# Kernel tuning notes

Measured on AMD Instinct MI355X. Metric: run time of the kernel, lower is better.

## Reference

```python
import jax, jax.numpy as jnp
import numpy as np

EPS = 1e-5

def _layer_norm(x, g, b):
    m = jnp.mean(x, axis=-1, keepdims=True)
    v = jnp.mean((x - m) ** 2, axis=-1, keepdims=True)
    return (x - m) / jnp.sqrt(v + EPS) * g + b

def _dpb(idx, w0, b0, g1, be1, w1, b1, g2, be2, w2, b2, g3, be3, w3, b3):
    # idx: (n, dim, 1) -> (h, n, dim)
    h = idx @ w0 + b0                                   # (n, dim, D)
    h = jax.nn.relu(_layer_norm(h, g1, be1)) @ w1 + b1  # pos1
    h = jax.nn.relu(_layer_norm(h, g2, be2)) @ w2 + b2  # pos2
    h = jax.nn.relu(_layer_norm(h, g3, be3)) @ w3 + b3  # pos3 -> (n, dim, H)
    return jnp.transpose(h, (2, 0, 1))                  # (H, n, dim)

def setup_inputs() -> dict:
    key = jax.random.key(0)
    ks = jax.random.split(key, 6)
    B, H, N, DIM, D = 8, 16, 4096, 64, 64
    s = 0.02
    return {
        "x": jax.random.normal(ks[0], (B, H, N, DIM), jnp.float32),
        "w0": jax.random.normal(ks[1], (1, D), jnp.float32) * s,
        "b0": jnp.zeros((D,), jnp.float32),
        "g1": jnp.ones((D,), jnp.float32),
        "be1": jnp.zeros((D,), jnp.float32),
        "w1": jax.random.normal(ks[2], (D, D), jnp.float32) * s,
        "b1": jnp.zeros((D,), jnp.float32),
        "g2": jnp.ones((D,), jnp.float32),
        "be2": jnp.zeros((D,), jnp.float32),
        "w2": jax.random.normal(ks[3], (D, D), jnp.float32) * s,
        "b2": jnp.zeros((D,), jnp.float32),
        "g3": jnp.ones((D,), jnp.float32),
        "be3": jnp.zeros((D,), jnp.float32),
        "w3": jax.random.normal(ks[4], (D, H), jnp.float32) * s,
        "b3": jnp.zeros((H,), jnp.float32),
    }

def reference(x, w0, b0, g1, be1, w1, b1, g2, be2, w2, b2, g3, be3, w3, b3):
    # DynamicToepliztMultiheadV3 forward (par_type=1, no pad/exp/decay, non-causal)
    n = x.shape[-2]
    dim = x.shape[-1]
    m = n - 1
    dpb_args = (w0, b0, g1, be1, w1, b1, g2, be2, w2, b2, g3, be3, w3, b3)
    scale = 1.0 / (m * dim)
    flat = jnp.arange(1, 1 + m * dim, dtype=x.dtype)
    pos_idx = (flat * scale).reshape(m, dim, 1)
    neg_idx = (-jnp.flip(flat) * scale).reshape(m, dim, 1)  # flip on flat, then reshape (matches torch)
    zero_idx = jnp.zeros((1, dim, 1), x.dtype)
    zero = _dpb(zero_idx, *dpb_args)   # (H, 1, dim)
    pos = _dpb(pos_idx, *dpb_args)     # (H, n-1, dim)
    neg = _dpb(neg_idx, *dpb_args)     # (H, n-1, dim)
    a = jnp.concatenate([zero, pos, zero, neg], axis=1)  # (H, 2n, dim)
    # FFT-based circular (Toeplitz) convolution along seq axis
    y = jnp.fft.rfft(x, 2 * n, axis=-2, norm='ortho')          # (B,H,n+1,dim) complex
    v = jnp.fft.rfft(a, axis=-2)[None]                          # backward norm, as in torch
    out = jnp.fft.irfft(v * y, 2 * n, axis=-2, norm='ortho')[:, :, :n, :]
    return out
```

## Files before the change

kernel.cpp:

```cpp
#include <hip/hip_runtime.h>
#include <math.h>

static const size_t OFF_TW = 0;
static const size_t OFF_V  = 32768;
static const size_t OFF_AT = OFF_V  + (size_t)16 * 64 * 4104 * 8;
static const size_t OFF_ZX = OFF_AT + (size_t)16 * 32 * 8192 * 8;
static const size_t WS_NEED = OFF_ZX + (size_t)128 * 32 * 4096 * 8;

__global__ void __launch_bounds__(256) k_init_tw(float2* __restrict__ tw)
{
    int k = blockIdx.x * 256 + threadIdx.x;
    if (k < 4096) {
        double a = (double)k * (3.14159265358979323846 / 4096.0);
        tw[k] = make_float2((float)cos(a), (float)(-sin(a)));
    }
}

__device__ __forceinline__ void ln_relu_arr(float* b,
                                            const float* __restrict__ g,
                                            const float* __restrict__ be)
{
    float s0 = 0, s1 = 0, s2 = 0, s3 = 0;
    #pragma unroll
    for (int k = 0; k < 64; k += 4) {
        s0 += b[k]; s1 += b[k + 1]; s2 += b[k + 2]; s3 += b[k + 3];
    }
    float m = (s0 + s1 + s2 + s3) * (1.0f / 64.0f);
    float v0 = 0, v1 = 0, v2 = 0, v3 = 0;
    #pragma unroll
    for (int k = 0; k < 64; k += 4) {
        float c0 = b[k] - m, c1 = b[k + 1] - m, c2 = b[k + 2] - m, c3 = b[k + 3] - m;
        v0 = fmaf(c0, c0, v0); v1 = fmaf(c1, c1, v1);
        v2 = fmaf(c2, c2, v2); v3 = fmaf(c3, c3, v3);
    }
    float inv = rsqrtf((v0 + v1 + v2 + v3) * (1.0f / 64.0f) + 1e-5f);
    #pragma unroll
    for (int k = 0; k < 64; ++k)
        b[k] = fmaxf(fmaf((b[k] - m) * inv, g[k], be[k]), 0.0f);
}

__device__ __forceinline__ void matmul64(const float* b, float* o,
                                         const float* __restrict__ w,
                                         const float* __restrict__ bias)
{
    #pragma unroll
    for (int j = 0; j < 64; ++j) o[j] = bias[j];
    #pragma unroll
    for (int k = 0; k < 64; ++k) {
        float bk = b[k];
        const float* wr = w + (k << 6);
        #pragma unroll
        for (int j = 0; j < 64; ++j) o[j] = fmaf(bk, wr[j], o[j]);
    }
}

__global__ void __launch_bounds__(256) k_dpb(
    const float* __restrict__ w0,  const float* __restrict__ b0,
    const float* __restrict__ g1,  const float* __restrict__ be1,
    const float* __restrict__ w1,  const float* __restrict__ b1,
    const float* __restrict__ g2,  const float* __restrict__ be2,
    const float* __restrict__ w2,  const float* __restrict__ b2,
    const float* __restrict__ g3,  const float* __restrict__ be3,
    const float* __restrict__ w3,  const float* __restrict__ b3,
    float* __restrict__ aTf)
{
    int e  = blockIdx.x * 256 + threadIdx.x;
    int r  = e & 8191;
    int dd = e >> 13;
    const float scale = (float)(1.0 / 262080.0);
    float u;
    if (r == 0 || r == 4096) u = 0.0f;
    else if (r < 4096)       u = (float)((r - 1) * 64 + dd + 1) * scale;
    else                     u = -(float)(262080 - ((r - 4097) * 64 + dd)) * scale;

    float b[64], o[64];
    #pragma unroll
    for (int j = 0; j < 64; ++j) b[j] = fmaf(u, w0[j], b0[j]);

    ln_relu_arr(b, g1, be1);
    matmul64(b, o, w1, b1);
    ln_relu_arr(o, g2, be2);
    matmul64(o, b, w2, b2);
    ln_relu_arr(b, g3, be3);

    float f[16];
    #pragma unroll
    for (int j = 0; j < 16; ++j) f[j] = b3[j];
    #pragma unroll
    for (int k = 0; k < 64; ++k) {
        float bk = b[k];
        const float* wr = w3 + (k << 4);
        #pragma unroll
        for (int j = 0; j < 16; ++j) f[j] = fmaf(bk, wr[j], f[j]);
    }
    #pragma unroll
    for (int h = 0; h < 16; ++h) {
        size_t idx = ((size_t)((h << 5) + (dd >> 1)) * 8192 + r) * 2 + (dd & 1);
        aTf[idx] = f[h];
    }
}

__device__ __forceinline__ int sw(int a)
{
    return a ^ ((a >> 4) & 15) ^ ((a >> 8) & 1);
}

__device__ __forceinline__ float2 cmul(float2 a, float2 b)
{
    return make_float2(fmaf(a.x, b.x, -(a.y * b.y)), fmaf(a.x, b.y, a.y * b.x));
}

template<bool INV>
__device__ __forceinline__ float2 twm(float2 a, float wr, float wi)
{
    float i = INV ? -wi : wi;
    return make_float2(fmaf(a.x, wr, -(a.y * i)), fmaf(a.x, i, a.y * wr));
}

template<bool INV>
__device__ __forceinline__ void fft8(float2* z)
{
    const float SQ = 0.70710678118654752440f;
    #pragma unroll
    for (int b = 0; b < 8; b += 2) {
        float2 u = z[b], t = z[b + 1];
        z[b]     = make_float2(u.x + t.x, u.y + t.y);
        z[b + 1] = make_float2(u.x - t.x, u.y - t.y);
    }
    const float w4r[2] = {1.0f, 0.0f};
    const float w4i[2] = {0.0f, -1.0f};
    #pragma unroll
    for (int b = 0; b < 8; b += 4) {
        #pragma unroll
        for (int j = 0; j < 2; ++j) {
            float2 u = z[b + j];
            float2 t = twm<INV>(z[b + j + 2], w4r[j], w4i[j]);
            z[b + j]     = make_float2(u.x + t.x, u.y + t.y);
            z[b + j + 2] = make_float2(u.x - t.x, u.y - t.y);
        }
    }
    const float w8r[4] = {1.0f, SQ, 0.0f, -SQ};
    const float w8i[4] = {0.0f, -SQ, -1.0f, -SQ};
    #pragma unroll
    for (int j = 0; j < 4; ++j) {
        float2 u = z[j];
        float2 t = twm<INV>(z[j + 4], w8r[j], w8i[j]);
        z[j]     = make_float2(u.x + t.x, u.y + t.y);
        z[j + 4] = make_float2(u.x - t.x, u.y - t.y);
    }
}

template<bool INV>
__device__ __forceinline__ void r8(float2* __restrict__ Z, int base, int j, int L, int s,
                                   const float2* __restrict__ tw)
{
    int addr[8];
    #pragma unroll
    for (int m = 0; m < 8; ++m) addr[m] = sw(base + j + L * m);
    float2 t1 = tw[j * s], t2 = tw[2 * j * s], t4 = tw[4 * j * s];
    if (INV) { t1.y = -t1.y; t2.y = -t2.y; t4.y = -t4.y; }
    float2 T3 = cmul(t1, t2), T5 = cmul(t1, t4), T6 = cmul(t2, t4), T7 = cmul(T3, t4);
    float2 z[8];
    z[0] = Z[addr[0]];
    z[1] = cmul(Z[addr[1]], t4);
    z[2] = cmul(Z[addr[2]], t2);
    z[3] = cmul(Z[addr[3]], T6);
    z[4] = cmul(Z[addr[4]], t1);
    z[5] = cmul(Z[addr[5]], T5);
    z[6] = cmul(Z[addr[6]], T3);
    z[7] = cmul(Z[addr[7]], T7);
    fft8<INV>(z);
    #pragma unroll
    for (int q = 0; q < 8; ++q) Z[addr[q]] = z[q];
}

template<int L, bool INV>
__device__ __forceinline__ void reg_stage16(float* xr, float* xi,
                                            const float2* __restrict__ tw)
{
    #pragma unroll
    for (int b = 0; b < 16; b += 2 * L) {
        #pragma unroll
        for (int j = 0; j < L; ++j) {
            float2 w = tw[j * (4096 / L)];
            float wr = w.x, wi = INV ? -w.y : w.y;
            int i0 = b + j, i1 = b + j + L;
            float tr = xr[i1] * wr - xi[i1] * wi;
            float ti = xr[i1] * wi + xi[i1] * wr;
            xr[i1] = xr[i0] - tr; xi[i1] = xi[i0] - ti;
            xr[i0] += tr;         xi[i0] += ti;
        }
    }
}

template<bool INV>
__device__ __forceinline__ void fft8192_lds(float2* __restrict__ Z,
                                            const float2* __restrict__ tw)
{
    const int t  = threadIdx.x;
    const int r9 = (int)(__brev((unsigned)t) >> 23);
    float xr[16], xi[16];
    #pragma unroll
    for (int i = 0; i < 16; ++i) {
        int r4 = (int)(__brev((unsigned)i) >> 28);
        float2 v = Z[sw((r4 << 9) | r9)];
        xr[i] = v.x; xi[i] = v.y;
    }
    __syncthreads();
    reg_stage16<1, INV>(xr, xi, tw);
    reg_stage16<2, INV>(xr, xi, tw);
    reg_stage16<4, INV>(xr, xi, tw);
    reg_stage16<8, INV>(xr, xi, tw);
    #pragma unroll
    for (int i = 0; i < 16; ++i) Z[sw(16 * t + i)] = make_float2(xr[i], xi[i]);
    __syncthreads();
    r8<INV>(Z, (t >> 4) * 128, t & 15, 16, 64, tw);
    r8<INV>(Z, ((t + 512) >> 4) * 128, t & 15, 16, 64, tw);
    __syncthreads();
    r8<INV>(Z, (t >> 7) * 1024, t & 127, 128, 8, tw);
    r8<INV>(Z, ((t + 512) >> 7) * 1024, (t + 512) & 127, 128, 8, tw);
    __syncthreads();
    r8<INV>(Z, 0, t, 1024, 1, tw);
    r8<INV>(Z, 0, t + 512, 1024, 1, tw);
    __syncthreads();
}

__global__ void __launch_bounds__(512, 4) k_vfft(const float2* __restrict__ aT,
                                                 const float2* __restrict__ tw,
                                                 float2* __restrict__ V)
{
    __shared__ float2 Z[8192];
    int blk = blockIdx.x;
    int h = blk >> 5, p = blk & 31;
    const float2* ac = aT + (size_t)(h * 32 + p) * 8192;
    int t = threadIdx.x;
    #pragma unroll
    for (int i = 0; i < 16; ++i) {
        int idx = i * 512 + t;
        Z[sw(idx)] = ac[idx];
    }
    __syncthreads();
    fft8192_lds<false>(Z, tw);
    const float s = 1.0f / 8192.0f;
    float2* V0 = V + (size_t)(h * 64 + 2 * p) * 4104;
    float2* V1 = V0 + 4104;
    for (int k = t; k <= 4096; k += 512) {
        int km = (8192 - k) & 8191;
        float2 z1 = Z[sw(k)], z2 = Z[sw(km)];
        float zr1 = z1.x, zi1 = z1.y;
        float zr2 = z2.x, zi2 = -z2.y;
        float a0r = 0.5f * (zr1 + zr2), a0i = 0.5f * (zi1 + zi2);
        float a1r = 0.5f * (zi1 - zi2), a1i = -0.5f * (zr1 - zr2);
        V0[k] = make_float2(a0r * s, a0i * s);
        V1[k] = make_float2(a1r * s, a1i * s);
    }
}

__global__ void __launch_bounds__(256) k_pack_x(const float* __restrict__ x,
                                                float2* __restrict__ zx)
{
    int blk = blockIdx.x;
    int bh = blk >> 7, rt = blk & 127, r0 = rt << 5;
    __shared__ float tile[64][33];
    const float* xp = x + (size_t)bh * 4096 * 64;
    int tid = threadIdx.x;
    #pragma unroll
    for (int i = 0; i < 8; ++i) {
        int idx = i * 256 + tid;
        int rr = idx >> 6, d = idx & 63;
        tile[d][rr] = xp[(size_t)(r0 + rr) * 64 + d];
    }
    __syncthreads();
    float2* zp = zx + (size_t)bh * 32 * 4096;
    #pragma unroll
    for (int i = 0; i < 4; ++i) {
        int idx = i * 256 + tid;
        int p = idx >> 5, rr = idx & 31;
        zp[(size_t)p * 4096 + r0 + rr] = make_float2(tile[2 * p][rr], tile[2 * p + 1][rr]);
    }
}

__global__ void __launch_bounds__(512, 4) k_conv(float2* __restrict__ zx,
                                                 const float2* __restrict__ V,
                                                 const float2* __restrict__ tw)
{
    __shared__ float2 Z[8192];
    int blk = blockIdx.x;
    int bh = blk >> 5, p = blk & 31, h = bh & 15;
    float2* zc = zx + (size_t)blk * 4096;
    int t = threadIdx.x;
    #pragma unroll
    for (int i = 0; i < 8; ++i) {
        int idx = i * 512 + t;
        Z[sw(idx)] = zc[idx];
        Z[sw(idx + 4096)] = make_float2(0.0f, 0.0f);
    }
    __syncthreads();
    fft8192_lds<false>(Z, tw);
    const float2* V0 = V + (size_t)(h * 64 + 2 * p) * 4104;
    const float2* V1 = V0 + 4104;
    for (int k = t; k <= 4096; k += 512) {
        int km = (8192 - k) & 8191;
        float2 z1 = Z[sw(k)], z2 = Z[sw(km)];
        float zr1 = z1.x, zi1 = z1.y;
        float zr2 = z2.x, zi2 = -z2.y;
        float x0r = 0.5f * (zr1 + zr2), x0i = 0.5f * (zi1 + zi2);
        float x1r = 0.5f * (zi1 - zi2), x1i = -0.5f * (zr1 - zr2);
        float2 v0 = V0[k], v1 = V1[k];
        float y0r = v0.x * x0r - v0.y * x0i, y0i = v0.x * x0i + v0.y * x0r;
        float y1r = v1.x * x1r - v1.y * x1i, y1i = v1.x * x1i + v1.y * x1r;
        Z[sw(k)] = make_float2(y0r - y1i, y0i + y1r);
        if (k > 0 && k < 4096)
            Z[sw(km)] = make_float2(y0r + y1i, y1r - y0i);
    }
    __syncthreads();
    fft8192_lds<true>(Z, tw);
    #pragma unroll
    for (int i = 0; i < 8; ++i) {
        int idx = i * 512 + t;
        zc[idx] = Z[sw(idx)];
    }
}

__global__ void __launch_bounds__(256) k_unpack_out(const float2* __restrict__ zo,
                                                    float* __restrict__ out)
{
    int blk = blockIdx.x;
    int bh = blk >> 7, rt = blk & 127, r0 = rt << 5;
    __shared__ float tile[64][33];
    const float2* zp = zo + (size_t)bh * 32 * 4096;
    int tid = threadIdx.x;
    #pragma unroll
    for (int i = 0; i < 4; ++i) {
        int idx = i * 256 + tid;
        int p = idx >> 5, rr = idx & 31;
        float2 v = zp[(size_t)p * 4096 + r0 + rr];
        tile[2 * p][rr] = v.x; tile[2 * p + 1][rr] = v.y;
    }
    __syncthreads();
    float* op = out + (size_t)bh * 4096 * 64;
    #pragma unroll
    for (int i = 0; i < 8; ++i) {
        int idx = i * 256 + tid;
        int rr = idx >> 6, d = idx & 63;
        op[(size_t)(r0 + rr) * 64 + d] = tile[d][rr];
    }
}

extern "C" void kernel_launch(void* const* d_in, const int* in_sizes, int n_in,
                              void* d_out, int out_size, void* d_ws, size_t ws_size,
                              hipStream_t stream)
{
    (void)in_sizes; (void)n_in; (void)out_size;
    const float* x   = (const float*)d_in[0];
    const float* w0  = (const float*)d_in[1];
    const float* b0  = (const float*)d_in[2];
    const float* g1  = (const float*)d_in[3];
    const float* be1 = (const float*)d_in[4];
    const float* w1  = (const float*)d_in[5];
    const float* b1  = (const float*)d_in[6];
    const float* g2  = (const float*)d_in[7];
    const float* be2 = (const float*)d_in[8];
    const float* w2  = (const float*)d_in[9];
    const float* b2  = (const float*)d_in[10];
    const float* g3  = (const float*)d_in[11];
    const float* be3 = (const float*)d_in[12];
    const float* w3  = (const float*)d_in[13];
    const float* b3  = (const float*)d_in[14];
    float* out = (float*)d_out;
    char* ws = (char*)d_ws;
    if (ws_size < WS_NEED) return;

    float2* tw = (float2*)(ws + OFF_TW);
    float2* V  = (float2*)(ws + OFF_V);
    float2* aT = (float2*)(ws + OFF_AT);
    float2* zx = (float2*)(ws + OFF_ZX);

    k_init_tw<<<16, 256, 0, stream>>>(tw);
    k_dpb<<<2048, 256, 0, stream>>>(w0, b0, g1, be1, w1, b1, g2, be2,
                                    w2, b2, g3, be3, w3, b3, (float*)aT);
    k_vfft<<<512, 512, 0, stream>>>(aT, tw, V);
    k_pack_x<<<16384, 256, 0, stream>>>(x, zx);
    k_conv<<<4096, 512, 0, stream>>>(zx, V, tw);
    k_unpack_out<<<16384, 256, 0, stream>>>((const float2*)zx, out);
}
```

Measured before the change: 779.5 us.

## Restructure 8192-point LDS FFT for 1024 threads and exploit zero padding

The in-LDS FFT is reworked from 512 threads with 16 register points each to 1024 threads with 8 register points each. It uses a new stage schedule: a radix-8 register pass, three radix-8 LDS passes, and a final radix-2 pass. In the forward conv FFT, the zero upper half is no longer written to shared memory. Instead, the first butterfly stage is skipped by duplicating the loaded values in registers. The goal is to cut LDS traffic and arithmetic and raise per-block parallelism, but launch_bounds(1024,1) may limit occupancy and changes register pressure.

```diff
diff --git a/kernel.cpp b/kernel.cpp
--- a/kernel.cpp
+++ b/kernel.cpp
@@ -175,11 +175,11 @@
 }
 
 template<int L, bool INV>
-__device__ __forceinline__ void reg_stage16(float* xr, float* xi,
-                                            const float2* __restrict__ tw)
-{
-    #pragma unroll
-    for (int b = 0; b < 16; b += 2 * L) {
+__device__ __forceinline__ void reg_stage8(float* xr, float* xi,
+                                           const float2* __restrict__ tw)
+{
+    #pragma unroll
+    for (int b = 0; b < 8; b += 2 * L) {
         #pragma unroll
         for (int j = 0; j < L; ++j) {
             float2 w = tw[j * (4096 / L)];
@@ -193,41 +193,60 @@
     }
 }
 
-template<bool INV>
+template<bool INV, bool PAD>
 __device__ __forceinline__ void fft8192_lds(float2* __restrict__ Z,
                                             const float2* __restrict__ tw)
 {
-    const int t  = threadIdx.x;
-    const int r9 = (int)(__brev((unsigned)t) >> 23);
-    float xr[16], xi[16];
-    #pragma unroll
-    for (int i = 0; i < 16; ++i) {
-        int r4 = (int)(__brev((unsigned)i) >> 28);
-        float2 v = Z[sw((r4 << 9) | r9)];
-        xr[i] = v.x; xi[i] = v.y;
-    }
-    __syncthreads();
-    reg_stage16<1, INV>(xr, xi, tw);
-    reg_stage16<2, INV>(xr, xi, tw);
-    reg_stage16<4, INV>(xr, xi, tw);
-    reg_stage16<8, INV>(xr, xi, tw);
-    #pragma unroll
-    for (int i = 0; i < 16; ++i) Z[sw(16 * t + i)] = make_float2(xr[i], xi[i]);
-    __syncthreads();
-    r8<INV>(Z, (t >> 4) * 128, t & 15, 16, 64, tw);
-    r8<INV>(Z, ((t + 512) >> 4) * 128, t & 15, 16, 64, tw);
-    __syncthreads();
-    r8<INV>(Z, (t >> 7) * 1024, t & 127, 128, 8, tw);
-    r8<INV>(Z, ((t + 512) >> 7) * 1024, (t + 512) & 127, 128, 8, tw);
-    __syncthreads();
-    r8<INV>(Z, 0, t, 1024, 1, tw);
-    r8<INV>(Z, 0, t + 512, 1024, 1, tw);
-    __syncthreads();
-}
-
-__global__ void __launch_bounds__(512, 4) k_vfft(const float2* __restrict__ aT,
-                                                 const float2* __restrict__ tw,
-                                                 float2* __restrict__ V)
+    const int t   = threadIdx.x;
+    const int r10 = (int)(__brev((unsigned)t) >> 22);
+    float xr[8], xi[8];
+    if (PAD) {
+        #pragma unroll
+        for (int i = 0; i < 8; i += 2) {
+            int r3 = (int)(__brev((unsigned)i) >> 29);
+            float2 v = Z[sw((r3 << 10) | r10)];
+            xr[i] = v.x; xi[i] = v.y;
+            xr[i + 1] = v.x; xi[i + 1] = v.y;
+        }
+    } else {
+        #pragma unroll
+        for (int i = 0; i < 8; ++i) {
+            int r3 = (int)(__brev((unsigned)i) >> 29);
+            float2 v = Z[sw((r3 << 10) | r10)];
+            xr[i] = v.x; xi[i] = v.y;
+        }
+    }
+    __syncthreads();
+    if (!PAD) reg_stage8<1, INV>(xr, xi, tw);
+    reg_stage8<2, INV>(xr, xi, tw);
+    reg_stage8<4, INV>(xr, xi, tw);
+    #pragma unroll
+    for (int i = 0; i < 8; ++i) Z[sw(8 * t + i)] = make_float2(xr[i], xi[i]);
+    __syncthreads();
+    r8<INV>(Z, (t >> 3) * 64, t & 7, 8, 128, tw);
+    __syncthreads();
+    r8<INV>(Z, (t >> 6) * 512, t & 63, 64, 16, tw);
+    __syncthreads();
+    r8<INV>(Z, (t >> 9) * 4096, t & 511, 512, 2, tw);
+    __syncthreads();
+    #pragma unroll
+    for (int m = 0; m < 4; ++m) {
+        int k = t + 1024 * m;
+        float2 w = tw[k];
+        float wi = INV ? -w.y : w.y;
+        int aL = sw(k), aH = sw(k + 4096);
+        float2 u = Z[aL], v = Z[aH];
+        float tr = fmaf(v.x, w.x, -(v.y * wi));
+        float ti = fmaf(v.x, wi, v.y * w.x);
+        Z[aL] = make_float2(u.x + tr, u.y + ti);
+        Z[aH] = make_float2(u.x - tr, u.y - ti);
+    }
+    __syncthreads();
+}
+
+__global__ void __launch_bounds__(1024, 1) k_vfft(const float2* __restrict__ aT,
+                                                  const float2* __restrict__ tw,
+                                                  float2* __restrict__ V)
 {
     __shared__ float2 Z[8192];
     int blk = blockIdx.x;
@@ -235,16 +254,16 @@
     const float2* ac = aT + (size_t)(h * 32 + p) * 8192;
     int t = threadIdx.x;
     #pragma unroll
-    for (int i = 0; i < 16; ++i) {
-        int idx = i * 512 + t;
+    for (int i = 0; i < 8; ++i) {
+        int idx = i * 1024 + t;
         Z[sw(idx)] = ac[idx];
     }
     __syncthreads();
-    fft8192_lds<false>(Z, tw);
+    fft8192_lds<false, false>(Z, tw);
     const float s = 1.0f / 8192.0f;
     float2* V0 = V + (size_t)(h * 64 + 2 * p) * 4104;
     float2* V1 = V0 + 4104;
-    for (int k = t; k <= 4096; k += 512) {
+    for (int k = t; k <= 4096; k += 1024) {
         int km = (8192 - k) & 8191;
         float2 z1 = Z[sw(k)], z2 = Z[sw(km)];
         float zr1 = z1.x, zi1 = z1.y;
@@ -280,9 +299,9 @@
     }
 }
 
-__global__ void __launch_bounds__(512, 4) k_conv(float2* __restrict__ zx,
-                                                 const float2* __restrict__ V,
-                                                 const float2* __restrict__ tw)
+__global__ void __launch_bounds__(1024, 1) k_conv(float2* __restrict__ zx,
+                                                  const float2* __restrict__ V,
+                                                  const float2* __restrict__ tw)
 {
     __shared__ float2 Z[8192];
     int blk = blockIdx.x;
@@ -290,16 +309,15 @@
     float2* zc = zx + (size_t)blk * 4096;
     int t = threadIdx.x;
     #pragma unroll
-    for (int i = 0; i < 8; ++i) {
-        int idx = i * 512 + t;
+    for (int i = 0; i < 4; ++i) {
+        int idx = i * 1024 + t;
         Z[sw(idx)] = zc[idx];
-        Z[sw(idx + 4096)] = make_float2(0.0f, 0.0f);
-    }
-    __syncthreads();
-    fft8192_lds<false>(Z, tw);
+    }
+    __syncthreads();
+    fft8192_lds<false, true>(Z, tw);
     const float2* V0 = V + (size_t)(h * 64 + 2 * p) * 4104;
     const float2* V1 = V0 + 4104;
-    for (int k = t; k <= 4096; k += 512) {
+    for (int k = t; k <= 4096; k += 1024) {
         int km = (8192 - k) & 8191;
         float2 z1 = Z[sw(k)], z2 = Z[sw(km)];
         float zr1 = z1.x, zi1 = z1.y;
@@ -314,10 +332,10 @@
             Z[sw(km)] = make_float2(y0r + y1i, y1r - y0i);
     }
     __syncthreads();
-    fft8192_lds<true>(Z, tw);
-    #pragma unroll
-    for (int i = 0; i < 8; ++i) {
-        int idx = i * 512 + t;
+    fft8192_lds<true, false>(Z, tw);
+    #pragma unroll
+    for (int i = 0; i < 4; ++i) {
+        int idx = i * 1024 + t;
         zc[idx] = Z[sw(idx)];
     }
 }
@@ -379,8 +397,8 @@
     k_init_tw<<<16, 256, 0, stream>>>(tw);
     k_dpb<<<2048, 256, 0, stream>>>(w0, b0, g1, be1, w1, b1, g2, be2,
                                     w2, b2, g3, be3, w3, b3, (float*)aT);
-    k_vfft<<<512, 512, 0, stream>>>(aT, tw, V);
+    k_vfft<<<512, 1024, 0, stream>>>(aT, tw, V);
     k_pack_x<<<16384, 256, 0, stream>>>(x, zx);
-    k_conv<<<4096, 512, 0, stream>>>(zx, V, tw);
+    k_conv<<<4096, 1024, 0, stream>>>(zx, V, tw);
     k_unpack_out<<<16384, 256, 0, stream>>>((const float2*)zx, out);
 }
```

New measurement: 770.7 us. About the same (-1.1%).

## Split 8192-point FFTs into even/odd 4096-point halves and stage DPB rows in LDS

Applied to the files above, without the earlier changes.

The 8192-point zero-padded FFTs in the convolution kernel become two 4096-point FFTs over the even and odd frequency bins. The odd-bin pass uses twiddle pre-multiplication, so the padded half is never transformed, and the inverse results are recombined with twiddles. This halves LDS use per block, though the kernel now runs four 4096-point FFTs and rereads its input. The V-spectrum kernel is split into even and odd blocks in the same way, and the DPB MLP stages activation rows in shared memory with smaller blocks to reduce register pressure.

```diff
diff --git a/kernel.cpp b/kernel.cpp
--- a/kernel.cpp
+++ b/kernel.cpp
@@ -39,22 +39,29 @@
         b[k] = fmaxf(fmaf((b[k] - m) * inv, g[k], be[k]), 0.0f);
 }
 
-__device__ __forceinline__ void matmul64(const float* b, float* o,
-                                         const float* __restrict__ w,
-                                         const float* __restrict__ bias)
-{
-    #pragma unroll
-    for (int j = 0; j < 64; ++j) o[j] = bias[j];
-    #pragma unroll
+__device__ __forceinline__ void store_row(float* __restrict__ row, const float* a)
+{
+    #pragma unroll
+    for (int k = 0; k < 64; ++k) row[k] = a[k];
+}
+
+template<int JN>
+__device__ __forceinline__ void matmul_lds(const float* __restrict__ row, float* o,
+                                           const float* __restrict__ w,
+                                           const float* __restrict__ bias)
+{
+    #pragma unroll
+    for (int j = 0; j < JN; ++j) o[j] = bias[j];
+    #pragma unroll 4
     for (int k = 0; k < 64; ++k) {
-        float bk = b[k];
-        const float* wr = w + (k << 6);
+        float bk = row[k];
+        const float* wr = w + k * JN;
         #pragma unroll
-        for (int j = 0; j < 64; ++j) o[j] = fmaf(bk, wr[j], o[j]);
-    }
-}
-
-__global__ void __launch_bounds__(256) k_dpb(
+        for (int j = 0; j < JN; ++j) o[j] = fmaf(bk, wr[j], o[j]);
+    }
+}
+
+__global__ void __launch_bounds__(128) k_dpb(
     const float* __restrict__ w0,  const float* __restrict__ b0,
     const float* __restrict__ g1,  const float* __restrict__ be1,
     const float* __restrict__ w1,  const float* __restrict__ b1,
@@ -64,7 +71,10 @@
     const float* __restrict__ w3,  const float* __restrict__ b3,
     float* __restrict__ aTf)
 {
-    int e  = blockIdx.x * 256 + threadIdx.x;
+    __shared__ float rowbuf[128 * 65];
+    float* row = &rowbuf[threadIdx.x * 65];
+
+    int e  = blockIdx.x * 128 + threadIdx.x;
     int r  = e & 8191;
     int dd = e >> 13;
     const float scale = (float)(1.0 / 262080.0);
@@ -73,26 +83,20 @@
     else if (r < 4096)       u = (float)((r - 1) * 64 + dd + 1) * scale;
     else                     u = -(float)(262080 - ((r - 4097) * 64 + dd)) * scale;
 
-    float b[64], o[64];
-    #pragma unroll
-    for (int j = 0; j < 64; ++j) b[j] = fmaf(u, w0[j], b0[j]);
-
-    ln_relu_arr(b, g1, be1);
-    matmul64(b, o, w1, b1);
+    float a[64], o[64];
+    #pragma unroll
+    for (int j = 0; j < 64; ++j) a[j] = fmaf(u, w0[j], b0[j]);
+    ln_relu_arr(a, g1, be1);
+    store_row(row, a);
+    matmul_lds<64>(row, o, w1, b1);
     ln_relu_arr(o, g2, be2);
-    matmul64(o, b, w2, b2);
-    ln_relu_arr(b, g3, be3);
-
+    store_row(row, o);
+    matmul_lds<64>(row, a, w2, b2);
+    ln_relu_arr(a, g3, be3);
+    store_row(row, a);
     float f[16];
-    #pragma unroll
-    for (int j = 0; j < 16; ++j) f[j] = b3[j];
-    #pragma unroll
-    for (int k = 0; k < 64; ++k) {
-        float bk = b[k];
-        const float* wr = w3 + (k << 4);
-        #pragma unroll
-        for (int j = 0; j < 16; ++j) f[j] = fmaf(bk, wr[j], f[j]);
-    }
+    matmul_lds<16>(row, f, w3, b3);
+
     #pragma unroll
     for (int h = 0; h < 16; ++h) {
         size_t idx = ((size_t)((h << 5) + (dd >> 1)) * 8192 + r) * 2 + (dd & 1);
@@ -175,11 +179,11 @@
 }
 
 template<int L, bool INV>
-__device__ __forceinline__ void reg_stage16(float* xr, float* xi,
-                                            const float2* __restrict__ tw)
-{
-    #pragma unroll
-    for (int b = 0; b < 16; b += 2 * L) {
+__device__ __forceinline__ void reg_stage8(float* xr, float* xi,
+                                           const float2* __restrict__ tw)
+{
+    #pragma unroll
+    for (int b = 0; b < 8; b += 2 * L) {
         #pragma unroll
         for (int j = 0; j < L; ++j) {
             float2 w = tw[j * (4096 / L)];
@@ -194,65 +198,81 @@
 }
 
 template<bool INV>
-__device__ __forceinline__ void fft8192_lds(float2* __restrict__ Z,
+__device__ __forceinline__ void fft4096_lds(float2* __restrict__ Z,
                                             const float2* __restrict__ tw)
 {
     const int t  = threadIdx.x;
     const int r9 = (int)(__brev((unsigned)t) >> 23);
-    float xr[16], xi[16];
-    #pragma unroll
-    for (int i = 0; i < 16; ++i) {
-        int r4 = (int)(__brev((unsigned)i) >> 28);
-        float2 v = Z[sw((r4 << 9) | r9)];
+    float xr[8], xi[8];
+    #pragma unroll
+    for (int i = 0; i < 8; ++i) {
+        int r3 = (int)(__brev((unsigned)i) >> 29);
+        float2 v = Z[sw((r3 << 9) | r9)];
         xr[i] = v.x; xi[i] = v.y;
     }
     __syncthreads();
-    reg_stage16<1, INV>(xr, xi, tw);
-    reg_stage16<2, INV>(xr, xi, tw);
-    reg_stage16<4, INV>(xr, xi, tw);
-    reg_stage16<8, INV>(xr, xi, tw);
-    #pragma unroll
-    for (int i = 0; i < 16; ++i) Z[sw(16 * t + i)] = make_float2(xr[i], xi[i]);
-    __syncthreads();
-    r8<INV>(Z, (t >> 4) * 128, t & 15, 16, 64, tw);
-    r8<INV>(Z, ((t + 512) >> 4) * 128, t & 15, 16, 64, tw);
-    __syncthreads();
-    r8<INV>(Z, (t >> 7) * 1024, t & 127, 128, 8, tw);
-    r8<INV>(Z, ((t + 512) >> 7) * 1024, (t + 512) & 127, 128, 8, tw);
-    __syncthreads();
-    r8<INV>(Z, 0, t, 1024, 1, tw);
-    r8<INV>(Z, 0, t + 512, 1024, 1, tw);
-    __syncthreads();
-}
-
-__global__ void __launch_bounds__(512, 4) k_vfft(const float2* __restrict__ aT,
+    reg_stage8<1, INV>(xr, xi, tw);
+    reg_stage8<2, INV>(xr, xi, tw);
+    reg_stage8<4, INV>(xr, xi, tw);
+    #pragma unroll
+    for (int i = 0; i < 8; ++i) Z[sw(8 * t + i)] = make_float2(xr[i], xi[i]);
+    __syncthreads();
+    r8<INV>(Z, (t >> 3) * 64, t & 7, 8, 128, tw);
+    __syncthreads();
+    r8<INV>(Z, (t >> 6) * 512, t & 63, 64, 16, tw);
+    __syncthreads();
+    r8<INV>(Z, 0, t, 512, 2, tw);
+    __syncthreads();
+}
+
+__global__ void __launch_bounds__(512, 3) k_vfft(const float2* __restrict__ aT,
                                                  const float2* __restrict__ tw,
                                                  float2* __restrict__ V)
 {
-    __shared__ float2 Z[8192];
+    __shared__ float2 Z[4096];
     int blk = blockIdx.x;
-    int h = blk >> 5, p = blk & 31;
-    const float2* ac = aT + (size_t)(h * 32 + p) * 8192;
+    int pair = blk >> 1, eo = blk & 1;
+    int h = pair >> 5, p = pair & 31;
+    const float2* ac = aT + (size_t)pair * 8192;
     int t = threadIdx.x;
-    #pragma unroll
-    for (int i = 0; i < 16; ++i) {
-        int idx = i * 512 + t;
-        Z[sw(idx)] = ac[idx];
-    }
-    __syncthreads();
-    fft8192_lds<false>(Z, tw);
+    if (eo == 0) {
+        #pragma unroll
+        for (int i = 0; i < 8; ++i) {
+            int idx = i * 512 + t;
+            float2 a = ac[idx], b = ac[idx + 4096];
+            Z[sw(idx)] = make_float2(a.x + b.x, a.y + b.y);
+        }
+    } else {
+        #pragma unroll
+        for (int i = 0; i < 8; ++i) {
+            int idx = i * 512 + t;
+            float2 a = ac[idx], b = ac[idx + 4096];
+            Z[sw(idx)] = cmul(make_float2(a.x - b.x, a.y - b.y), tw[idx]);
+        }
+    }
+    __syncthreads();
+    fft4096_lds<false>(Z, tw);
     const float s = 1.0f / 8192.0f;
     float2* V0 = V + (size_t)(h * 64 + 2 * p) * 4104;
     float2* V1 = V0 + 4104;
-    for (int k = t; k <= 4096; k += 512) {
-        int km = (8192 - k) & 8191;
-        float2 z1 = Z[sw(k)], z2 = Z[sw(km)];
-        float zr1 = z1.x, zi1 = z1.y;
-        float zr2 = z2.x, zi2 = -z2.y;
-        float a0r = 0.5f * (zr1 + zr2), a0i = 0.5f * (zi1 + zi2);
-        float a1r = 0.5f * (zi1 - zi2), a1i = -0.5f * (zr1 - zr2);
-        V0[k] = make_float2(a0r * s, a0i * s);
-        V1[k] = make_float2(a1r * s, a1i * s);
+    if (eo == 0) {
+        for (int j = t; j <= 2048; j += 512) {
+            int jm = (4096 - j) & 4095;
+            float2 z1 = Z[sw(j)], z2 = Z[sw(jm)];
+            float zr1 = z1.x, zi1 = z1.y;
+            float zr2 = z2.x, zi2 = -z2.y;
+            V0[2 * j] = make_float2(0.5f * (zr1 + zr2) * s, 0.5f * (zi1 + zi2) * s);
+            V1[2 * j] = make_float2(0.5f * (zi1 - zi2) * s, -0.5f * (zr1 - zr2) * s);
+        }
+    } else {
+        for (int j = t; j < 2048; j += 512) {
+            int jm = 4095 - j;
+            float2 z1 = Z[sw(j)], z2 = Z[sw(jm)];
+            float zr1 = z1.x, zi1 = z1.y;
+            float zr2 = z2.x, zi2 = -z2.y;
+            V0[2 * j + 1] = make_float2(0.5f * (zr1 + zr2) * s, 0.5f * (zi1 + zi2) * s);
+            V1[2 * j + 1] = make_float2(0.5f * (zi1 - zi2) * s, -0.5f * (zr1 - zr2) * s);
+        }
     }
 }
 
@@ -280,45 +300,79 @@
     }
 }
 
-__global__ void __launch_bounds__(512, 4) k_conv(float2* __restrict__ zx,
+__global__ void __launch_bounds__(512, 3) k_conv(float2* __restrict__ zx,
                                                  const float2* __restrict__ V,
                                                  const float2* __restrict__ tw)
 {
-    __shared__ float2 Z[8192];
+    __shared__ float2 Z[4096];
     int blk = blockIdx.x;
     int bh = blk >> 5, p = blk & 31, h = bh & 15;
     float2* zc = zx + (size_t)blk * 4096;
     int t = threadIdx.x;
+    const float2* V0 = V + (size_t)(h * 64 + 2 * p) * 4104;
+    const float2* V1 = V0 + 4104;
+
     #pragma unroll
     for (int i = 0; i < 8; ++i) {
         int idx = i * 512 + t;
         Z[sw(idx)] = zc[idx];
-        Z[sw(idx + 4096)] = make_float2(0.0f, 0.0f);
-    }
-    __syncthreads();
-    fft8192_lds<false>(Z, tw);
-    const float2* V0 = V + (size_t)(h * 64 + 2 * p) * 4104;
-    const float2* V1 = V0 + 4104;
-    for (int k = t; k <= 4096; k += 512) {
-        int km = (8192 - k) & 8191;
-        float2 z1 = Z[sw(k)], z2 = Z[sw(km)];
+    }
+    __syncthreads();
+    fft4096_lds<false>(Z, tw);
+    for (int j = t; j <= 2048; j += 512) {
+        int jm = (4096 - j) & 4095;
+        float2 z1 = Z[sw(j)], z2 = Z[sw(jm)];
         float zr1 = z1.x, zi1 = z1.y;
         float zr2 = z2.x, zi2 = -z2.y;
         float x0r = 0.5f * (zr1 + zr2), x0i = 0.5f * (zi1 + zi2);
         float x1r = 0.5f * (zi1 - zi2), x1i = -0.5f * (zr1 - zr2);
-        float2 v0 = V0[k], v1 = V1[k];
+        float2 v0 = V0[2 * j], v1 = V1[2 * j];
         float y0r = v0.x * x0r - v0.y * x0i, y0i = v0.x * x0i + v0.y * x0r;
         float y1r = v1.x * x1r - v1.y * x1i, y1i = v1.x * x1i + v1.y * x1r;
-        Z[sw(k)] = make_float2(y0r - y1i, y0i + y1r);
-        if (k > 0 && k < 4096)
-            Z[sw(km)] = make_float2(y0r + y1i, y1r - y0i);
-    }
-    __syncthreads();
-    fft8192_lds<true>(Z, tw);
+        Z[sw(j)] = make_float2(y0r - y1i, y0i + y1r);
+        if (j > 0 && j < 2048)
+            Z[sw(jm)] = make_float2(y0r + y1i, y1r - y0i);
+    }
+    __syncthreads();
+    fft4096_lds<true>(Z, tw);
+    float er[8], ei[8];
+    #pragma unroll
+    for (int i = 0; i < 8; ++i) {
+        float2 v = Z[sw(i * 512 + t)];
+        er[i] = v.x; ei[i] = v.y;
+    }
+    __syncthreads();
+
     #pragma unroll
     for (int i = 0; i < 8; ++i) {
         int idx = i * 512 + t;
-        zc[idx] = Z[sw(idx)];
+        Z[sw(idx)] = cmul(zc[idx], tw[idx]);
+    }
+    __syncthreads();
+    fft4096_lds<false>(Z, tw);
+    for (int j = t; j < 2048; j += 512) {
+        int jm = 4095 - j;
+        float2 z1 = Z[sw(j)], z2 = Z[sw(jm)];
+        float zr1 = z1.x, zi1 = z1.y;
+        float zr2 = z2.x, zi2 = -z2.y;
+        float x0r = 0.5f * (zr1 + zr2), x0i = 0.5f * (zi1 + zi2);
+        float x1r = 0.5f * (zi1 - zi2), x1i = -0.5f * (zr1 - zr2);
+        float2 v0 = V0[2 * j + 1], v1 = V1[2 * j + 1];
+        float y0r = v0.x * x0r - v0.y * x0i, y0i = v0.x * x0i + v0.y * x0r;
+        float y1r = v1.x * x1r - v1.y * x1i, y1i = v1.x * x1i + v1.y * x1r;
+        Z[sw(j)]  = make_float2(y0r - y1i, y0i + y1r);
+        Z[sw(jm)] = make_float2(y0r + y1i, y1r - y0i);
+    }
+    __syncthreads();
+    fft4096_lds<true>(Z, tw);
+    #pragma unroll
+    for (int i = 0; i < 8; ++i) {
+        int idx = i * 512 + t;
+        float2 o = Z[sw(idx)];
+        float2 w = tw[idx];
+        float yr = er[i] + (w.x * o.x + w.y * o.y);
+        float yi = ei[i] + (w.x * o.y - w.y * o.x);
+        zc[idx] = make_float2(yr, yi);
     }
 }
 
@@ -377,9 +431,9 @@
     float2* zx = (float2*)(ws + OFF_ZX);
 
     k_init_tw<<<16, 256, 0, stream>>>(tw);
-    k_dpb<<<2048, 256, 0, stream>>>(w0, b0, g1, be1, w1, b1, g2, be2,
+    k_dpb<<<4096, 128, 0, stream>>>(w0, b0, g1, be1, w1, b1, g2, be2,
                                     w2, b2, g3, be3, w3, b3, (float*)aT);
-    k_vfft<<<512, 512, 0, stream>>>(aT, tw, V);
+    k_vfft<<<1024, 512, 0, stream>>>(aT, tw, V);
     k_pack_x<<<16384, 256, 0, stream>>>(x, zx);
     k_conv<<<4096, 512, 0, stream>>>(zx, V, tw);
     k_unpack_out<<<16384, 256, 0, stream>>>((const float2*)zx, out);
```

Result: slower. 824.9 us (+5.8%).
